# Kernel optimization log

Measured on AMD Instinct MI355X. Metric: run time of the kernel, lower is better.

The kernel has to match this reference:

```python
import jax, jax.numpy as jnp
import numpy as np

B, NCH, T = 4096, 8, 128
F1, F2 = 16, 32          # nChan*2, nChan*4
TP = 60                  # (128 - 10)//2 + 1 after enhanced block
FEAT = 2 * TP * F2       # 3840, matches nn.BatchNorm1d(3840)
NCLS = 12
HG = 4 * F2              # stacked LSTM gate rows (i,f,g,o)
EPS = 1e-5


def setup_inputs():
    key = jax.random.key(0)
    ks = jax.random.split(key, 24)
    n = lambda i, sh, s=0.1: jax.random.normal(ks[i], sh, dtype=jnp.float32) * s
    return {
        "x": jax.random.normal(ks[0], (B, 1, NCH, T), dtype=jnp.float32),
        "template": jax.random.normal(ks[1], (B, 1, NCH, T), dtype=jnp.float32),
        "conv1_w": n(2, (F1, 1, NCH, 1)),
        "conv1_b": n(3, (F1,)),
        "bn1_g": jnp.ones((F1,), jnp.float32),
        "bn1_b": jnp.zeros((F1,), jnp.float32),
        "prelu1": jnp.full((1,), 0.25, jnp.float32),
        "conv2_w": n(4, (F2, F1, 1, 10)),
        "conv2_b": n(5, (F2,)),
        "bn2_g": jnp.ones((F2,), jnp.float32),
        "bn2_b": jnp.zeros((F2,), jnp.float32),
        "prelu2": jnp.full((1,), 0.25, jnp.float32),
        "wih_f": n(6, (HG, F2)), "whh_f": n(7, (HG, F2)),
        "bih_f": n(8, (HG,)), "bhh_f": n(9, (HG,)),
        "wih_r": n(10, (HG, F2)), "whh_r": n(11, (HG, F2)),
        "bih_r": n(12, (HG,)), "bhh_r": n(13, (HG,)),
        "bnf_g": jnp.ones((FEAT,), jnp.float32),
        "bnf_b": jnp.zeros((FEAT,), jnp.float32),
        "convf_w": n(14, (1, 1, 5, 1)),
        "convf_b": n(15, (1,)),
    }


def _conv2d(x, w, b, stride=(1, 1), padding=((0, 0), (0, 0))):
    y = jax.lax.conv_general_dilated(x, w, window_strides=stride, padding=padding,
                                     dimension_numbers=("NCHW", "OIHW", "NCHW"))
    return y + b[None, :, None, None]


def _bn2d(x, g, b):  # training-mode batch stats over (N,H,W), biased var
    m = jnp.mean(x, axis=(0, 2, 3), keepdims=True)
    v = jnp.mean((x - m) ** 2, axis=(0, 2, 3), keepdims=True)
    return (x - m) * jax.lax.rsqrt(v + EPS) * g[None, :, None, None] + b[None, :, None, None]


def _bn1d(x, g, b):  # x: (N, FEAT)
    m = jnp.mean(x, axis=0, keepdims=True)
    v = jnp.mean((x - m) ** 2, axis=0, keepdims=True)
    return (x - m) * jax.lax.rsqrt(v + EPS) * g[None, :] + b[None, :]


def _prelu(x, a):
    return jnp.where(x >= 0, x, a * x)


def _lstm_dir(x, wih, whh, bih, bhh):  # x: (T, B, I) -> (T, B, H)
    Hh = whh.shape[1]
    Bn = x.shape[1]

    def step(carry, xt):
        h, c = carry
        gates = xt @ wih.T + h @ whh.T + bih + bhh  # (B, 4H), torch gate order i,f,g,o
        i, f, g, o = jnp.split(gates, 4, axis=-1)
        c = jax.nn.sigmoid(f) * c + jax.nn.sigmoid(i) * jnp.tanh(g)
        h = jax.nn.sigmoid(o) * jnp.tanh(c)
        return (h, c), h

    init = (jnp.zeros((Bn, Hh), x.dtype), jnp.zeros((Bn, Hh), x.dtype))
    _, hs = jax.lax.scan(step, init, x)
    return hs


def _rnn(xbct, wih_f, whh_f, bih_f, bhh_f, wih_r, whh_r, bih_r, bhh_r):
    # Faithful to torch: x.view(T, -1, c) is a raw row-major reshape of the
    # contiguous (b, c, T) buffer, NOT a transpose.
    b, c, Tn = xbct.shape
    xi = xbct.reshape(Tn, b, c)
    fwd = _lstm_dir(xi, wih_f, whh_f, bih_f, bhh_f)
    bwd = _lstm_dir(xi[::-1], wih_r, whh_r, bih_r, bhh_r)[::-1]
    r = jnp.concatenate([fwd, bwd], axis=-1)  # (T, b, 2c)
    return r.reshape(b, 2 * Tn * c, 1)        # raw reshape, matches r_out.view


def _forward(x, template, conv1_w, conv1_b, bn1_g, bn1_b, prelu1,
             conv2_w, conv2_b, bn2_g, bn2_b, prelu2,
             wih_f, whh_f, bih_f, bhh_f, wih_r, whh_r, bih_r, bhh_r,
             bnf_g, bnf_b, convf_w, convf_b):
    lstm_p = (wih_f, whh_f, bih_f, bhh_f, wih_r, whh_r, bih_r, bhh_r)

    def branch(inp):
        h = _conv2d(inp, conv1_w, conv1_b)               # (B, 16, 1, 128)
        h = _prelu(_bn2d(h, bn1_g, bn1_b), prelu1)
        h = _conv2d(h, conv2_w, conv2_b, stride=(1, 2))  # (B, 32, 1, 60)
        h = _prelu(_bn2d(h, bn2_g, bn2_b), prelu2)
        out_sig = h[:, :, 0, :]                          # (B, 32, 60)
        r1 = _rnn(out_sig, *lstm_p)
        # Original: numpy FFT round-trip -> detached, float cast keeps real part.
        fftm = jnp.real(jnp.fft.fft(jax.lax.stop_gradient(out_sig), axis=-1)).astype(inp.dtype)
        r2 = _rnn(fftm, *lstm_p)
        sig = (r1 + r2).reshape(-1, FEAT)                # (B, 3840)
        return _bn1d(sig, bnf_g, bnf_b)

    sig = branch(x)
    tpt = branch(template)

    x_ = sig.reshape(-1, 320, NCLS)
    t_ = tpt.reshape(-1, 320, NCLS)
    corr_xt = jnp.sum(x_ * t_, axis=1)
    corr_xx = jnp.sum(x_ * x_, axis=1)
    corr_tt = jnp.sum(t_ * t_, axis=1)
    corr = corr_xt / jnp.sqrt(corr_tt) / jnp.sqrt(corr_xx)  # (B, 12)

    o = corr.reshape(-1, NCLS, 1, 1)
    o = jnp.transpose(o, (0, 2, 1, 3))                      # (B, 1, 12, 1)
    o = _conv2d(o, convf_w, convf_b, padding=((2, 2), (0, 0)))
    out = o.reshape(-1, NCLS)
    return out, corr


def reference(x, template, conv1_w, conv1_b, bn1_g, bn1_b, prelu1,
              conv2_w, conv2_b, bn2_g, bn2_b, prelu2,
              wih_f, whh_f, bih_f, bhh_f, wih_r, whh_r, bih_r, bhh_r,
              bnf_g, bnf_b, convf_w, convf_b):
    return _forward(x, template, conv1_w, conv1_b, bn1_g, bn1_b, prelu1,
                    conv2_w, conv2_b, bn2_g, bn2_b, prelu2,
                    wih_f, whh_f, bih_f, bhh_f, wih_r, whh_r, bih_r, bhh_r,
                    bnf_g, bnf_b, convf_w, convf_b)
```

## Files before the change

### kernel.cpp

```cpp
#include <hip/hip_runtime.h>
#include <math.h>

#define EPS 1e-5f

typedef __attribute__((ext_vector_type(8))) short bf16x8;
typedef __attribute__((ext_vector_type(4))) float f32x4;
typedef __attribute__((ext_vector_type(4))) short s16x4;

__device__ __forceinline__ float fast_rcp(float x){ return __builtin_amdgcn_rcpf(x); }
__device__ __forceinline__ float sigf(float x){ return fast_rcp(1.0f + __expf(-x)); }
__device__ __forceinline__ float tanhfast(float x){ return fmaf(2.0f, fast_rcp(1.0f + __expf(-2.0f*x)), -1.0f); }
__device__ __forceinline__ float dot4(float4 a, float4 b, float c){
  return fmaf(a.w,b.w, fmaf(a.z,b.z, fmaf(a.y,b.y, fmaf(a.x,b.x, c))));
}
__device__ __forceinline__ short f2bf(float f){
  unsigned u = __float_as_uint(f);
  u = (u + 0x7FFFu + ((u>>16)&1u)) >> 16;
  return (short)u;
}
__device__ __forceinline__ float bf2f(short s){
  return __uint_as_float(((unsigned)(unsigned short)s) << 16);
}

__global__ __launch_bounds__(256) void k_conv1_stats(
    const float* __restrict__ x, const float* __restrict__ w1,
    const float* __restrict__ b1, float* __restrict__ part)
{
  __shared__ float red[4][32];
  float s[16], q[16];
#pragma unroll
  for (int f=0; f<16; ++f) { s[f]=0.f; q[f]=0.f; }
  float w1r[128];
#pragma unroll
  for (int i=0; i<128; ++i) w1r[i] = w1[i];
  float b1r[16];
#pragma unroll
  for (int f=0; f<16; ++f) b1r[f] = b1[f];
  const int tid = threadIdx.x;
  for (int iter=0; iter<8; ++iter) {
    int n = blockIdx.x*2048 + iter*256 + tid;
    int b = n >> 7, t = n & 127;
    const float* xb = x + b*1024 + t;
    float xv[8];
#pragma unroll
    for (int ch=0; ch<8; ++ch) xv[ch] = xb[ch*128];
#pragma unroll
    for (int f=0; f<16; ++f) {
      float v = b1r[f];
#pragma unroll
      for (int ch=0; ch<8; ++ch) v = fmaf(xv[ch], w1r[f*8+ch], v);
      s[f] += v; q[f] = fmaf(v,v,q[f]);
    }
  }
#pragma unroll
  for (int f=0; f<16; ++f) {
#pragma unroll
    for (int d=32; d>0; d>>=1) { s[f] += __shfl_down(s[f],d); q[f] += __shfl_down(q[f],d); }
  }
  const int lane = tid & 63, wv = tid >> 6;
  if (lane == 0) {
#pragma unroll
    for (int f=0; f<16; ++f) { red[wv][2*f] = s[f]; red[wv][2*f+1] = q[f]; }
  }
  __syncthreads();
  if (tid < 32) {
    float v = red[0][tid] + red[1][tid] + red[2][tid] + red[3][tid];
    part[blockIdx.x*32 + tid] = v;
  }
}

__global__ __launch_bounds__(256) void k_reduce_finalize(
    const float* __restrict__ part, int nblk, int C,
    const float* __restrict__ g, const float* __restrict__ b,
    float* __restrict__ prm, float invN)
{
  __shared__ float red[4][2];
  const int c = blockIdx.x;
  const int tid = threadIdx.x;
  float s=0.f, q=0.f;
  for (int i=tid; i<nblk; i+=256) {
    s += part[(size_t)i*2*C + 2*c];
    q += part[(size_t)i*2*C + 2*c + 1];
  }
#pragma unroll
  for (int d=32; d>0; d>>=1) { s += __shfl_down(s,d); q += __shfl_down(q,d); }
  const int lane = tid & 63, wv = tid >> 6;
  if (lane==0) { red[wv][0]=s; red[wv][1]=q; }
  __syncthreads();
  if (tid==0) {
    s = red[0][0]+red[1][0]+red[2][0]+red[3][0];
    q = red[0][1]+red[1][1]+red[2][1]+red[3][1];
    float m = s*invN;
    float v = q*invN - m*m;
    float sc = g[c] / sqrtf(v + EPS);
    prm[2*c]   = sc;
    prm[2*c+1] = fmaf(-m, sc, b[c]);
  }
}

__global__ __launch_bounds__(256) void k_conv2(
    const float* __restrict__ x,
    const float* __restrict__ w1, const float* __restrict__ b1,
    const float* __restrict__ prm1, const float* __restrict__ prelu1,
    const float* __restrict__ w2, const float* __restrict__ b2,
    float* __restrict__ sig, float* __restrict__ part2)
{
  __shared__ float xb[1024];
  __shared__ float h1p[16*136];
  __shared__ float w2s[32*16*12];
  __shared__ float w1s[128];
  __shared__ float p1s[32];
  int tid = threadIdx.x; int b = blockIdx.x;
  *(float4*)&xb[tid*4] = *(const float4*)&x[b*1024 + tid*4];
  for (int i=tid; i<5120; i+=256) { int ff=i/10, k=i-ff*10; w2s[ff*12+k] = w2[i]; }
  if (tid<128) w1s[tid] = w1[tid];
  if (tid<32)  p1s[tid] = prm1[tid];
  float a1 = prelu1[0];
  __syncthreads();
#pragma unroll
  for (int r=0; r<8; ++r) {
    int o = tid + 256*r; int f = o>>7, t = o&127;
    float v = b1[f];
#pragma unroll
    for (int ch=0; ch<8; ++ch) v = fmaf(xb[ch*128+t], w1s[f*8+ch], v);
    v = fmaf(v, p1s[2*f], p1s[2*f+1]);
    v = (v>=0.f) ? v : a1*v;
    h1p[f*136 + t] = v;
  }
  __syncthreads();
  int f2 = tid>>3, wb = (tid&7)*8;
  float acc[8];
  float bb = b2[f2];
#pragma unroll
  for (int j=0;j<8;++j) acc[j]=bb;
  for (int f1=0; f1<16; ++f1) {
    const float* hrow = &h1p[f1*136 + 2*wb];
    float hw[24];
#pragma unroll
    for (int m=0;m<6;++m) *(float4*)&hw[m*4] = *(const float4*)&hrow[m*4];
    const float* wr = &w2s[(f2*16+f1)*12];
    float wk[10];
    *(float4*)&wk[0] = *(const float4*)&wr[0];
    *(float4*)&wk[4] = *(const float4*)&wr[4];
    wk[8]=wr[8]; wk[9]=wr[9];
#pragma unroll
    for (int j=0;j<8;++j)
#pragma unroll
      for (int k=0;k<10;++k) acc[j] = fmaf(hw[2*j+k], wk[k], acc[j]);
  }
  float s=0.f, q=0.f;
#pragma unroll
  for (int j=0;j<8;++j) {
    int w = wb+j;
    if (w < 60) { sig[b*1920 + f2*60 + w] = acc[j]; s += acc[j]; q = fmaf(acc[j],acc[j],q); }
  }
  s += __shfl_down(s,4,8); q += __shfl_down(q,4,8);
  s += __shfl_down(s,2,8); q += __shfl_down(q,2,8);
  s += __shfl_down(s,1,8); q += __shfl_down(q,1,8);
  if ((tid&7)==0) {
    part2[(size_t)b*64 + 2*f2]     = s;
    part2[(size_t)b*64 + 2*f2 + 1] = q;
  }
}

__global__ void k_costab(float* __restrict__ ct)
{
  int i = blockIdx.x*256 + threadIdx.x;
  if (i < 3600) {
    int k = i/60, n = i - k*60;
    int m = (k*n) % 60;
    ct[i] = cosf(0.104719755119659775f * (float)m);
  }
}

__global__ __launch_bounds__(256) void k_sigfft(
    float* __restrict__ sig, float* __restrict__ fft,
    const float* __restrict__ prm2, const float* __restrict__ prelu2,
    const float* __restrict__ ctab)
{
  __shared__ float ct[3600];
  __shared__ float rowb[4][4][60];
  int tid = threadIdx.x;
  for (int i=tid; i<3600; i+=256) ct[i] = ctab[i];
  int r4 = tid>>6, lane = tid&63;
  float a2 = prelu2[0];
  __syncthreads();
#pragma unroll
  for (int it=0; it<4; ++it) {
    int row = blockIdx.x*16 + it*4 + r4;
    int c = row & 31;
    float sc = prm2[2*c], sh = prm2[2*c+1];
    size_t base = (size_t)row*60;
    if (lane < 60) {
      float v = fmaf(sig[base+lane], sc, sh);
      v = (v>=0.f) ? v : a2*v;
      rowb[it][r4][lane] = v;
      sig[base+lane] = v;
    }
    if (lane < 60) {
      float s = 0.f;
      const float* rb = rowb[it][r4];
#pragma unroll 6
      for (int n=0; n<60; ++n) s = fmaf(rb[n], ct[n*60+lane], s);
      fft[base+lane] = s;
    }
  }
}

__global__ __launch_bounds__(256) void k_xfrag(const float* __restrict__ src, short* __restrict__ frag)
{
  __shared__ float XS[64*33];
  const int tid = threadIdx.x;
  const int bid = blockIdx.x;
  const int t = bid >> 6, sblk = bid & 63;
  const float* sp = src + (size_t)t*131072 + (size_t)sblk*2048;
  {
    float4 v0 = *(const float4*)&sp[tid*8];
    float4 v1 = *(const float4*)&sp[tid*8 + 4];
    int s = tid >> 2, k = (tid & 3) * 8;
    float* d = &XS[s*33 + k];
    d[0]=v0.x; d[1]=v0.y; d[2]=v0.z; d[3]=v0.w;
    d[4]=v1.x; d[5]=v1.y; d[6]=v1.z; d[7]=v1.w;
  }
  __syncthreads();
  const int stile = tid >> 6, l = tid & 63;
  const int m = l & 15, g = l >> 4;
  const float* rp = &XS[(stile*16 + m)*33 + g*8];
  bf16x8 v;
#pragma unroll
  for (int j=0;j<8;++j) v[j] = f2bf(rp[j]);
  *(bf16x8*)(frag + ((size_t)(t*256 + sblk*4 + stile)*64 + l)*8) = v;
}

__global__ __launch_bounds__(256,1) void k_lstm_mfma(
    const short* __restrict__ fragSA, const short* __restrict__ fragFA,
    const short* __restrict__ fragSB, const short* __restrict__ fragFB,
    float* __restrict__ routA, float* __restrict__ routB,
    const float* __restrict__ wihf, const float* __restrict__ whhf,
    const float* __restrict__ bihf, const float* __restrict__ bhhf,
    const float* __restrict__ wihr, const float* __restrict__ whhr,
    const float* __restrict__ bihr, const float* __restrict__ bhhr,
    int zsel)
{
  __shared__ short hbuf[2][5120];
  const int tid = threadIdx.x;
  const int l = tid & 63, wv = tid >> 6;
  const int a = wv >> 1, ch = wv & 1;
  const int m = l & 15, g = l >> 4;
  const int sb = blockIdx.x * 64;
  const int dir = blockIdx.y;
  const int br = (gridDim.z == 2) ? blockIdx.z : zsel;
  const short* fragS = br ? fragSB : fragSA;
  const short* fragF = br ? fragFB : fragFA;
  float* out = br ? routB : routA;
  const float* wih = dir ? wihr : wihf;
  const float* whh = dir ? whhr : whhf;
  const float* bih = dir ? bihr : bihf;
  const float* bhh = dir ? bhhr : bhhf;

  bf16x8 Ax[4], Ah[4];
#pragma unroll
  for (int G=0; G<4; ++G) {
    const float* wr = wih + (size_t)(32*G + 16*a + m)*32 + 8*g;
    const float* hr = whh + (size_t)(32*G + 16*a + m)*32 + 8*g;
#pragma unroll
    for (int j=0;j<8;++j){ Ax[G][j]=f2bf(wr[j]); Ah[G][j]=f2bf(hr[j]); }
  }
  float bias[16];
#pragma unroll
  for (int G=0;G<4;++G)
#pragma unroll
    for (int r=0;r<4;++r){
      int row = 32*G + 16*a + 4*g + r;
      bias[G*4+r] = bih[row] + bhh[row];
    }
  for (int i=tid; i<2560; i+=256) ((int*)hbuf[1])[i] = 0;

  const short* fsrc = ch ? fragF : fragS;
  const int st0 = sb >> 4;
  const int tt0 = dir ? 59 : 0;
  bf16x8 bx[4];
#pragma unroll
  for (int ct=0; ct<4; ++ct)
    bx[ct] = *(const bf16x8*)(fsrc + ((size_t)(tt0*256 + st0 + ct)*64 + l)*8);

  float cst[16];
#pragma unroll
  for (int i=0;i<16;++i) cst[i]=0.f;

  __syncthreads();

#pragma unroll 2
  for (int q=0; q<60; ++q) {
    const int tt = dir ? (59-q) : q;
    const short* hrd = hbuf[(q+1)&1];
    bf16x8 bh[4];
#pragma unroll
    for (int ct=0; ct<4; ++ct)
      bh[ct] = *(const bf16x8*)(hrd + (64*ch + 16*ct + m)*40 + 8*g);
    bf16x8 bx2[4];
    if (q < 59) {
      const int tn = dir ? (58-q) : (q+1);
#pragma unroll
      for (int ct=0; ct<4; ++ct)
        bx2[ct] = *(const bf16x8*)(fsrc + ((size_t)(tn*256 + st0 + ct)*64 + l)*8);
    }
    f32x4 acc[16];
#pragma unroll
    for (int G=0; G<4; ++G) {
      f32x4 binit;
      binit[0]=bias[G*4]; binit[1]=bias[G*4+1]; binit[2]=bias[G*4+2]; binit[3]=bias[G*4+3];
#pragma unroll
      for (int ct=0; ct<4; ++ct) {
        f32x4 t0 = __builtin_amdgcn_mfma_f32_16x16x32_bf16(Ax[G], bx[ct], binit, 0,0,0);
        acc[G*4+ct] = __builtin_amdgcn_mfma_f32_16x16x32_bf16(Ah[G], bh[ct], t0, 0,0,0);
      }
    }
    short* hwr = hbuf[q&1];
#pragma unroll
    for (int ct=0; ct<4; ++ct) {
      s16x4 hv;
#pragma unroll
      for (int r=0; r<4; ++r) {
        float gi = acc[0*4+ct][r], gf = acc[1*4+ct][r];
        float gg = acc[2*4+ct][r], go = acc[3*4+ct][r];
        float c = sigf(gf)*cst[ct*4+r] + sigf(gi)*tanhfast(gg);
        cst[ct*4+r] = c;
        hv[r] = f2bf(sigf(go)*tanhfast(c));
      }
      *(s16x4*)(hwr + (64*ch + 16*ct + m)*40 + 16*a + 4*g) = hv;
    }
    __syncthreads();
#pragma unroll
    for (int i2=0; i2<2; ++i2) {
      int s = 32*ch + 16*i2 + m;
      const s16x4 h1 = *(const s16x4*)(hwr + s*40 + 16*a + 4*g);
      const s16x4 h2 = *(const s16x4*)(hwr + (64+s)*40 + 16*a + 4*g);
      float4 o;
      o.x = bf2f(h1[0])+bf2f(h2[0]);
      o.y = bf2f(h1[1])+bf2f(h2[1]);
      o.z = bf2f(h1[2])+bf2f(h2[2]);
      o.w = bf2f(h1[3])+bf2f(h2[3]);
      *(float4*)(out + (size_t)tt*262144 + (size_t)(sb+s)*64 + dir*32 + 16*a + 4*g) = o;
    }
#pragma unroll
    for (int ct=0; ct<4; ++ct) bx[ct] = bx2[ct];
  }
}

__global__ __launch_bounds__(256) void k_bnfstats(const float* __restrict__ rb, float* __restrict__ acc)
{
  int col = blockIdx.x*256 + threadIdx.x;
  size_t r0 = (size_t)blockIdx.y*256;
  const float* p = rb + r0*3840 + col;
  float s=0.f, q=0.f;
  for (int r=0; r<256; ++r) { float v = p[(size_t)r*3840]; s += v; q = fmaf(v,v,q); }
  atomicAdd(&acc[2*col], s); atomicAdd(&acc[2*col+1], q);
}

__global__ void k_finalize_bn(const float* __restrict__ acc, const float* __restrict__ g,
                              const float* __restrict__ b, float* __restrict__ prm,
                              int C, float invN)
{
  int i = blockIdx.x*blockDim.x + threadIdx.x;
  if (i < C) {
    float m = acc[2*i]*invN;
    float v = acc[2*i+1]*invN - m*m;
    float sc = g[i] / sqrtf(v + EPS);
    prm[2*i]   = sc;
    prm[2*i+1] = fmaf(-m, sc, b[i]);
  }
}

__global__ __launch_bounds__(64) void k_corr(
    const float* __restrict__ ra, const float* __restrict__ rb,
    const float* __restrict__ pfa, const float* __restrict__ pfb,
    const float* __restrict__ cw, const float* __restrict__ cb,
    float* __restrict__ dout)
{
  __shared__ float sxt[12], sxx[12], stt[12], cv[12];
  int lane = threadIdx.x; int r = blockIdx.x;
  if (lane < 12) { sxt[lane]=0.f; sxx[lane]=0.f; stt[lane]=0.f; }
  __syncthreads();
  const float* pa = ra + (size_t)r*3840;
  const float* pb = rb + (size_t)r*3840;
  float xt0=0,xx0=0,tt0=0, xt1=0,xx1=0,tt1=0, xt2=0,xx2=0,tt2=0;
  for (int i=0; i<60; i+=3) {
    { int fe = lane + 64*i;
      float a = fmaf(pa[fe], pfa[2*fe], pfa[2*fe+1]);
      float b = fmaf(pb[fe], pfb[2*fe], pfb[2*fe+1]);
      xt0 = fmaf(a,b,xt0); xx0 = fmaf(a,a,xx0); tt0 = fmaf(b,b,tt0); }
    { int fe = lane + 64*(i+1);
      float a = fmaf(pa[fe], pfa[2*fe], pfa[2*fe+1]);
      float b = fmaf(pb[fe], pfb[2*fe], pfb[2*fe+1]);
      xt1 = fmaf(a,b,xt1); xx1 = fmaf(a,a,xx1); tt1 = fmaf(b,b,tt1); }
    { int fe = lane + 64*(i+2);
      float a = fmaf(pa[fe], pfa[2*fe], pfa[2*fe+1]);
      float b = fmaf(pb[fe], pfb[2*fe], pfb[2*fe+1]);
      xt2 = fmaf(a,b,xt2); xx2 = fmaf(a,a,xx2); tt2 = fmaf(b,b,tt2); }
  }
  int c0 = lane % 12;
  int c1 = (c0+4) % 12;
  int c2 = (c0+8) % 12;
  atomicAdd(&sxt[c0], xt0); atomicAdd(&sxx[c0], xx0); atomicAdd(&stt[c0], tt0);
  atomicAdd(&sxt[c1], xt1); atomicAdd(&sxx[c1], xx1); atomicAdd(&stt[c1], tt1);
  atomicAdd(&sxt[c2], xt2); atomicAdd(&sxx[c2], xx2); atomicAdd(&stt[c2], tt2);
  __syncthreads();
  if (lane < 12) {
    float corr = sxt[lane] / sqrtf(stt[lane]) / sqrtf(sxx[lane]);
    cv[lane] = corr;
    dout[49152 + r*12 + lane] = corr;
  }
  __syncthreads();
  if (lane < 12) {
    float o = cb[0];
#pragma unroll
    for (int k=0; k<5; ++k) { int j = lane + k - 2; if (j>=0 && j<12) o = fmaf(cv[j], cw[k], o); }
    dout[r*12 + lane] = o;
  }
}

extern "C" void kernel_launch(void* const* d_in, const int* in_sizes, int n_in,
                              void* d_out, int out_size, void* d_ws, size_t ws_size,
                              hipStream_t stream)
{
  const float* x    = (const float*)d_in[0];
  const float* tpl  = (const float*)d_in[1];
  const float* w1   = (const float*)d_in[2];
  const float* b1   = (const float*)d_in[3];
  const float* g1   = (const float*)d_in[4];
  const float* bb1  = (const float*)d_in[5];
  const float* p1   = (const float*)d_in[6];
  const float* w2   = (const float*)d_in[7];
  const float* b2   = (const float*)d_in[8];
  const float* g2   = (const float*)d_in[9];
  const float* bb2  = (const float*)d_in[10];
  const float* p2   = (const float*)d_in[11];
  const float* wihf = (const float*)d_in[12];
  const float* whhf = (const float*)d_in[13];
  const float* bihf = (const float*)d_in[14];
  const float* bhhf = (const float*)d_in[15];
  const float* wihr = (const float*)d_in[16];
  const float* whhr = (const float*)d_in[17];
  const float* bihr = (const float*)d_in[18];
  const float* bhhr = (const float*)d_in[19];
  const float* gf   = (const float*)d_in[20];
  const float* bf   = (const float*)d_in[21];
  const float* cw   = (const float*)d_in[22];
  const float* cb   = (const float*)d_in[23];
  float* W   = (float*)d_ws;
  float* out = (float*)d_out;

  constexpr size_t PRM1A=64, PRM1B=96, PRM2A=256, PRM2B=320;
  constexpr size_t ACCFA=512, ACCFB=8192, PRMFA=15872, PRMFB=23552, CTAB=31232;
  constexpr size_t P1P=35072, P2P=43264;
  constexpr size_t SIGSZ = 7864320, RSZ = 15728640, FRAGF = 3932160;
  constexpr size_t BIG0 = 307200;
  constexpr size_t F_SIGA=BIG0, F_FFTA=F_SIGA+SIGSZ, F_SIGB=F_FFTA+SIGSZ, F_FFTB=F_SIGB+SIGSZ;
  constexpr size_t F_RBUFA=F_FFTB+SIGSZ, F_RBUFB=F_RBUFA+RSZ;
  constexpr size_t F_FR0=F_RBUFB+RSZ;
  constexpr size_t F_TOTAL=(F_FR0 + 4*FRAGF)*sizeof(float);
  constexpr size_t T_SIG=BIG0, T_FFT=T_SIG+SIGSZ, T_RBUFA=T_FFT+SIGSZ, T_RBUFB=T_RBUFA+RSZ;
  constexpr size_t T_FR0=T_RBUFB+RSZ;

  const bool fast = ws_size >= F_TOTAL;

  hipMemsetAsync(W, 0, 65536*sizeof(float)/sizeof(float)>0?262144:262144, stream);
  k_costab<<<15,256,0,stream>>>(W+CTAB);

  if (fast) {
    for (int br=0; br<2; ++br) {
      const float* xin  = br ? tpl : x;
      float* prm1 = W + (br ? PRM1B : PRM1A);
      float* prm2 = W + (br ? PRM2B : PRM2A);
      float* sig  = W + (br ? F_SIGB : F_SIGA);
      float* fft  = W + (br ? F_FFTB : F_FFTA);
      k_conv1_stats<<<256,256,0,stream>>>(xin, w1, b1, W+P1P);
      k_reduce_finalize<<<16,256,0,stream>>>(W+P1P, 256, 16, g1, bb1, prm1, 1.f/524288.f);
      k_conv2<<<4096,256,0,stream>>>(xin, w1, b1, prm1, p1, w2, b2, sig, W+P2P);
      k_reduce_finalize<<<32,256,0,stream>>>(W+P2P, 4096, 32, g2, bb2, prm2, 1.f/245760.f);
      k_sigfft<<<8192,256,0,stream>>>(sig, fft, prm2, p2, W+CTAB);
    }
    short* frSA = (short*)(W + F_FR0);
    short* frFA = (short*)(W + F_FR0 + FRAGF);
    short* frSB = (short*)(W + F_FR0 + 2*FRAGF);
    short* frFB = (short*)(W + F_FR0 + 3*FRAGF);
    k_xfrag<<<3840,256,0,stream>>>(W+F_SIGA, frSA);
    k_xfrag<<<3840,256,0,stream>>>(W+F_FFTA, frFA);
    k_xfrag<<<3840,256,0,stream>>>(W+F_SIGB, frSB);
    k_xfrag<<<3840,256,0,stream>>>(W+F_FFTB, frFB);
    k_lstm_mfma<<<dim3(64,2,2),256,0,stream>>>(frSA, frFA, frSB, frFB,
        W+F_RBUFA, W+F_RBUFB,
        wihf,whhf,bihf,bhhf, wihr,whhr,bihr,bhhr, 0);
    k_bnfstats<<<dim3(15,16),256,0,stream>>>(W+F_RBUFA, W+ACCFA);
    k_bnfstats<<<dim3(15,16),256,0,stream>>>(W+F_RBUFB, W+ACCFB);
    k_finalize_bn<<<15,256,0,stream>>>(W+ACCFA, gf, bf, W+PRMFA, 3840, 1.f/4096.f);
    k_finalize_bn<<<15,256,0,stream>>>(W+ACCFB, gf, bf, W+PRMFB, 3840, 1.f/4096.f);
    k_corr<<<4096,64,0,stream>>>(W+F_RBUFA, W+F_RBUFB, W+PRMFA, W+PRMFB, cw, cb, out);
  } else {
    short* frS = (short*)(W + T_FR0);
    short* frF = (short*)(W + T_FR0 + FRAGF);
    for (int br=0; br<2; ++br) {
      const float* xin  = br ? tpl : x;
      float* prm1 = W + (br ? PRM1B : PRM1A);
      float* prm2 = W + (br ? PRM2B : PRM2A);
      float* sig  = W + T_SIG;
      float* fft  = W + T_FFT;
      float* rbuf = W + (br ? T_RBUFB : T_RBUFA);
      k_conv1_stats<<<256,256,0,stream>>>(xin, w1, b1, W+P1P);
      k_reduce_finalize<<<16,256,0,stream>>>(W+P1P, 256, 16, g1, bb1, prm1, 1.f/524288.f);
      k_conv2<<<4096,256,0,stream>>>(xin, w1, b1, prm1, p1, w2, b2, sig, W+P2P);
      k_reduce_finalize<<<32,256,0,stream>>>(W+P2P, 4096, 32, g2, bb2, prm2, 1.f/245760.f);
      k_sigfft<<<8192,256,0,stream>>>(sig, fft, prm2, p2, W+CTAB);
      k_xfrag<<<3840,256,0,stream>>>(sig, frS);
      k_xfrag<<<3840,256,0,stream>>>(fft, frF);
      k_lstm_mfma<<<dim3(64,2,1),256,0,stream>>>(frS, frF, frS, frF,
          rbuf, rbuf, wihf,whhf,bihf,bhhf, wihr,whhr,bihr,bhhr, 0);
    }
    k_bnfstats<<<dim3(15,16),256,0,stream>>>(W+T_RBUFA, W+ACCFA);
    k_bnfstats<<<dim3(15,16),256,0,stream>>>(W+T_RBUFB, W+ACCFB);
    k_finalize_bn<<<15,256,0,stream>>>(W+ACCFA, gf, bf, W+PRMFA, 3840, 1.f/4096.f);
    k_finalize_bn<<<15,256,0,stream>>>(W+ACCFB, gf, bf, W+PRMFB, 3840, 1.f/4096.f);
    k_corr<<<4096,64,0,stream>>>(W+T_RBUFA, W+T_RBUFB, W+PRMFA, W+PRMFB, cw, cb, out);
  }
}
```

Baseline: 688.4 us.

## Restructure LSTM into single-wave blocks over 8-sequence tiles with shuffle-based sum

The LSTM kernel moves from 256-thread blocks, each covering 64 sequences with a block-wide barrier every step, to 64-thread single-wave blocks. Each wave covers 8 sig plus 8 fft sequences packed into one 16-column MFMA tile and computes all 8 gate row tiles. The sig+fft output sum now uses lane shuffles, which removes the LDS round trip and the __syncthreads per timestep. Fragment building is simplified to interleave sig and fft directly without LDS. In exchange, every wave recomputes the full weight fragments and the grid grows much larger, with each wave carrying a serial 60-step chain.

```diff
diff --git a/kernel.cpp b/kernel.cpp
--- a/kernel.cpp
+++ b/kernel.cpp
@@ -10,9 +10,6 @@
 __device__ __forceinline__ float fast_rcp(float x){ return __builtin_amdgcn_rcpf(x); }
 __device__ __forceinline__ float sigf(float x){ return fast_rcp(1.0f + __expf(-x)); }
 __device__ __forceinline__ float tanhfast(float x){ return fmaf(2.0f, fast_rcp(1.0f + __expf(-2.0f*x)), -1.0f); }
-__device__ __forceinline__ float dot4(float4 a, float4 b, float c){
-  return fmaf(a.w,b.w, fmaf(a.z,b.z, fmaf(a.y,b.y, fmaf(a.x,b.x, c))));
-}
 __device__ __forceinline__ short f2bf(float f){
   unsigned u = __float_as_uint(f);
   u = (u + 0x7FFFu + ((u>>16)&1u)) >> 16;
@@ -207,144 +204,108 @@
   }
 }
 
-__global__ __launch_bounds__(256) void k_xfrag(const float* __restrict__ src, short* __restrict__ frag)
-{
-  __shared__ float XS[64*33];
+__global__ __launch_bounds__(256) void k_xfrag2(
+    const float* __restrict__ sig, const float* __restrict__ fft,
+    short* __restrict__ frag)
+{
   const int tid = threadIdx.x;
-  const int bid = blockIdx.x;
-  const int t = bid >> 6, sblk = bid & 63;
-  const float* sp = src + (size_t)t*131072 + (size_t)sblk*2048;
-  {
-    float4 v0 = *(const float4*)&sp[tid*8];
-    float4 v1 = *(const float4*)&sp[tid*8 + 4];
-    int s = tid >> 2, k = (tid & 3) * 8;
-    float* d = &XS[s*33 + k];
-    d[0]=v0.x; d[1]=v0.y; d[2]=v0.z; d[3]=v0.w;
-    d[4]=v1.x; d[5]=v1.y; d[6]=v1.z; d[7]=v1.w;
-  }
-  __syncthreads();
-  const int stile = tid >> 6, l = tid & 63;
+  const int wv = tid >> 6, l = tid & 63;
+  const int id = blockIdx.x*4 + wv;
+  const int t = id >> 9, sg = id & 511;
   const int m = l & 15, g = l >> 4;
-  const float* rp = &XS[(stile*16 + m)*33 + g*8];
+  const float* src = (m < 8) ? sig : fft;
+  const float* p = src + (size_t)t*131072 + (size_t)(8*sg + (m&7))*32 + 8*g;
+  float4 v0 = *(const float4*)p;
+  float4 v1 = *(const float4*)(p+4);
   bf16x8 v;
-#pragma unroll
-  for (int j=0;j<8;++j) v[j] = f2bf(rp[j]);
-  *(bf16x8*)(frag + ((size_t)(t*256 + sblk*4 + stile)*64 + l)*8) = v;
-}
-
-__global__ __launch_bounds__(256,1) void k_lstm_mfma(
-    const short* __restrict__ fragSA, const short* __restrict__ fragFA,
-    const short* __restrict__ fragSB, const short* __restrict__ fragFB,
+  v[0]=f2bf(v0.x); v[1]=f2bf(v0.y); v[2]=f2bf(v0.z); v[3]=f2bf(v0.w);
+  v[4]=f2bf(v1.x); v[5]=f2bf(v1.y); v[6]=f2bf(v1.z); v[7]=f2bf(v1.w);
+  *(bf16x8*)(frag + ((size_t)id*64 + l)*8) = v;
+}
+
+__global__ __launch_bounds__(64,2) void k_lstm8(
+    const short* __restrict__ fragA, const short* __restrict__ fragB,
     float* __restrict__ routA, float* __restrict__ routB,
     const float* __restrict__ wihf, const float* __restrict__ whhf,
     const float* __restrict__ bihf, const float* __restrict__ bhhf,
     const float* __restrict__ wihr, const float* __restrict__ whhr,
-    const float* __restrict__ bihr, const float* __restrict__ bhhr,
-    int zsel)
-{
-  __shared__ short hbuf[2][5120];
-  const int tid = threadIdx.x;
-  const int l = tid & 63, wv = tid >> 6;
-  const int a = wv >> 1, ch = wv & 1;
+    const float* __restrict__ bihr, const float* __restrict__ bhhr)
+{
+  __shared__ short hb[640];
+  const int l = threadIdx.x & 63;
   const int m = l & 15, g = l >> 4;
-  const int sb = blockIdx.x * 64;
+  const int sg = blockIdx.x;
   const int dir = blockIdx.y;
-  const int br = (gridDim.z == 2) ? blockIdx.z : zsel;
-  const short* fragS = br ? fragSB : fragSA;
-  const short* fragF = br ? fragFB : fragFA;
+  const int br = blockIdx.z;
+  const short* frag = br ? fragB : fragA;
   float* out = br ? routB : routA;
   const float* wih = dir ? wihr : wihf;
   const float* whh = dir ? whhr : whhf;
   const float* bih = dir ? bihr : bihf;
   const float* bhh = dir ? bhhr : bhhf;
 
-  bf16x8 Ax[4], Ah[4];
-#pragma unroll
-  for (int G=0; G<4; ++G) {
-    const float* wr = wih + (size_t)(32*G + 16*a + m)*32 + 8*g;
-    const float* hr = whh + (size_t)(32*G + 16*a + m)*32 + 8*g;
-#pragma unroll
-    for (int j=0;j<8;++j){ Ax[G][j]=f2bf(wr[j]); Ah[G][j]=f2bf(hr[j]); }
-  }
-  float bias[16];
-#pragma unroll
-  for (int G=0;G<4;++G)
-#pragma unroll
-    for (int r=0;r<4;++r){
-      int row = 32*G + 16*a + 4*g + r;
-      bias[G*4+r] = bih[row] + bhh[row];
-    }
-  for (int i=tid; i<2560; i+=256) ((int*)hbuf[1])[i] = 0;
-
-  const short* fsrc = ch ? fragF : fragS;
-  const int st0 = sb >> 4;
+  bf16x8 Ax[8], Ah[8];
+#pragma unroll
+  for (int rt=0; rt<8; ++rt) {
+    const float* wr = wih + (size_t)(16*rt+m)*32 + 8*g;
+    const float* hr = whh + (size_t)(16*rt+m)*32 + 8*g;
+#pragma unroll
+    for (int j=0;j<8;++j){ Ax[rt][j]=f2bf(wr[j]); Ah[rt][j]=f2bf(hr[j]); }
+  }
+  f32x4 bias[8];
+#pragma unroll
+  for (int rt=0; rt<8; ++rt)
+#pragma unroll
+    for (int r=0;r<4;++r){ int R=16*rt+4*g+r; bias[rt][r]=bih[R]+bhh[R]; }
+
+  for (int i=l; i<320; i+=64) ((int*)hb)[i] = 0;
+
+  float cst[2][4];
+#pragma unroll
+  for (int h2=0;h2<2;++h2)
+#pragma unroll
+    for (int r=0;r<4;++r) cst[h2][r]=0.f;
+
   const int tt0 = dir ? 59 : 0;
-  bf16x8 bx[4];
-#pragma unroll
-  for (int ct=0; ct<4; ++ct)
-    bx[ct] = *(const bf16x8*)(fsrc + ((size_t)(tt0*256 + st0 + ct)*64 + l)*8);
-
-  float cst[16];
-#pragma unroll
-  for (int i=0;i<16;++i) cst[i]=0.f;
-
-  __syncthreads();
-
-#pragma unroll 2
+  bf16x8 bx = *(const bf16x8*)(frag + ((size_t)(tt0*512+sg)*64 + l)*8);
+
   for (int q=0; q<60; ++q) {
     const int tt = dir ? (59-q) : q;
-    const short* hrd = hbuf[(q+1)&1];
-    bf16x8 bh[4];
-#pragma unroll
-    for (int ct=0; ct<4; ++ct)
-      bh[ct] = *(const bf16x8*)(hrd + (64*ch + 16*ct + m)*40 + 8*g);
-    bf16x8 bx2[4];
+    bf16x8 bh = *(const bf16x8*)(hb + m*40 + 8*g);
+    bf16x8 bxn;
     if (q < 59) {
       const int tn = dir ? (58-q) : (q+1);
-#pragma unroll
-      for (int ct=0; ct<4; ++ct)
-        bx2[ct] = *(const bf16x8*)(fsrc + ((size_t)(tn*256 + st0 + ct)*64 + l)*8);
-    }
-    f32x4 acc[16];
-#pragma unroll
-    for (int G=0; G<4; ++G) {
-      f32x4 binit;
-      binit[0]=bias[G*4]; binit[1]=bias[G*4+1]; binit[2]=bias[G*4+2]; binit[3]=bias[G*4+3];
-#pragma unroll
-      for (int ct=0; ct<4; ++ct) {
-        f32x4 t0 = __builtin_amdgcn_mfma_f32_16x16x32_bf16(Ax[G], bx[ct], binit, 0,0,0);
-        acc[G*4+ct] = __builtin_amdgcn_mfma_f32_16x16x32_bf16(Ah[G], bh[ct], t0, 0,0,0);
+      bxn = *(const bf16x8*)(frag + ((size_t)(tn*512+sg)*64 + l)*8);
+    }
+    f32x4 acc[8];
+#pragma unroll
+    for (int rt=0; rt<8; ++rt) {
+      acc[rt] = __builtin_amdgcn_mfma_f32_16x16x32_bf16(Ax[rt], bx, bias[rt], 0,0,0);
+      acc[rt] = __builtin_amdgcn_mfma_f32_16x16x32_bf16(Ah[rt], bh, acc[rt], 0,0,0);
+    }
+#pragma unroll
+    for (int h2=0; h2<2; ++h2) {
+      s16x4 hv;
+      float hnf[4];
+#pragma unroll
+      for (int r=0; r<4; ++r) {
+        float gi = acc[h2][r],   gf = acc[2+h2][r];
+        float gg = acc[4+h2][r], go = acc[6+h2][r];
+        float cn = sigf(gf)*cst[h2][r] + sigf(gi)*tanhfast(gg);
+        cst[h2][r] = cn;
+        float hn = sigf(go)*tanhfast(cn);
+        hnf[r] = hn; hv[r] = f2bf(hn);
       }
-    }
-    short* hwr = hbuf[q&1];
-#pragma unroll
-    for (int ct=0; ct<4; ++ct) {
-      s16x4 hv;
-#pragma unroll
-      for (int r=0; r<4; ++r) {
-        float gi = acc[0*4+ct][r], gf = acc[1*4+ct][r];
-        float gg = acc[2*4+ct][r], go = acc[3*4+ct][r];
-        float c = sigf(gf)*cst[ct*4+r] + sigf(gi)*tanhfast(gg);
-        cst[ct*4+r] = c;
-        hv[r] = f2bf(sigf(go)*tanhfast(c));
-      }
-      *(s16x4*)(hwr + (64*ch + 16*ct + m)*40 + 16*a + 4*g) = hv;
-    }
-    __syncthreads();
-#pragma unroll
-    for (int i2=0; i2<2; ++i2) {
-      int s = 32*ch + 16*i2 + m;
-      const s16x4 h1 = *(const s16x4*)(hwr + s*40 + 16*a + 4*g);
-      const s16x4 h2 = *(const s16x4*)(hwr + (64+s)*40 + 16*a + 4*g);
+      *(s16x4*)(hb + m*40 + 16*h2 + 4*g) = hv;
       float4 o;
-      o.x = bf2f(h1[0])+bf2f(h2[0]);
-      o.y = bf2f(h1[1])+bf2f(h2[1]);
-      o.z = bf2f(h1[2])+bf2f(h2[2]);
-      o.w = bf2f(h1[3])+bf2f(h2[3]);
-      *(float4*)(out + (size_t)tt*262144 + (size_t)(sb+s)*64 + dir*32 + 16*a + 4*g) = o;
-    }
-#pragma unroll
-    for (int ct=0; ct<4; ++ct) bx[ct] = bx2[ct];
+      o.x = hnf[0] + __shfl_xor(hnf[0], 8);
+      o.y = hnf[1] + __shfl_xor(hnf[1], 8);
+      o.z = hnf[2] + __shfl_xor(hnf[2], 8);
+      o.w = hnf[3] + __shfl_xor(hnf[3], 8);
+      if (m < 8)
+        *(float4*)(out + (size_t)tt*262144 + (size_t)(8*sg+m)*64 + dir*32 + 16*h2 + 4*g) = o;
+    }
+    bx = bxn;
   }
 }
 
@@ -454,18 +415,18 @@
   constexpr size_t PRM1A=64, PRM1B=96, PRM2A=256, PRM2B=320;
   constexpr size_t ACCFA=512, ACCFB=8192, PRMFA=15872, PRMFB=23552, CTAB=31232;
   constexpr size_t P1P=35072, P2P=43264;
-  constexpr size_t SIGSZ = 7864320, RSZ = 15728640, FRAGF = 3932160;
+  constexpr size_t SIGSZ = 7864320, RSZ = 15728640, FRAGF = 7864320;
   constexpr size_t BIG0 = 307200;
   constexpr size_t F_SIGA=BIG0, F_FFTA=F_SIGA+SIGSZ, F_SIGB=F_FFTA+SIGSZ, F_FFTB=F_SIGB+SIGSZ;
   constexpr size_t F_RBUFA=F_FFTB+SIGSZ, F_RBUFB=F_RBUFA+RSZ;
   constexpr size_t F_FR0=F_RBUFB+RSZ;
-  constexpr size_t F_TOTAL=(F_FR0 + 4*FRAGF)*sizeof(float);
+  constexpr size_t F_TOTAL=(F_FR0 + 2*FRAGF)*sizeof(float);
   constexpr size_t T_SIG=BIG0, T_FFT=T_SIG+SIGSZ, T_RBUFA=T_FFT+SIGSZ, T_RBUFB=T_RBUFA+RSZ;
   constexpr size_t T_FR0=T_RBUFB+RSZ;
 
   const bool fast = ws_size >= F_TOTAL;
 
-  hipMemsetAsync(W, 0, 65536*sizeof(float)/sizeof(float)>0?262144:262144, stream);
+  hipMemsetAsync(W, 0, 262144, stream);
   k_costab<<<15,256,0,stream>>>(W+CTAB);
 
   if (fast) {
@@ -481,25 +442,19 @@
       k_reduce_finalize<<<32,256,0,stream>>>(W+P2P, 4096, 32, g2, bb2, prm2, 1.f/245760.f);
       k_sigfft<<<8192,256,0,stream>>>(sig, fft, prm2, p2, W+CTAB);
     }
-    short* frSA = (short*)(W + F_FR0);
-    short* frFA = (short*)(W + F_FR0 + FRAGF);
-    short* frSB = (short*)(W + F_FR0 + 2*FRAGF);
-    short* frFB = (short*)(W + F_FR0 + 3*FRAGF);
-    k_xfrag<<<3840,256,0,stream>>>(W+F_SIGA, frSA);
-    k_xfrag<<<3840,256,0,stream>>>(W+F_FFTA, frFA);
-    k_xfrag<<<3840,256,0,stream>>>(W+F_SIGB, frSB);
-    k_xfrag<<<3840,256,0,stream>>>(W+F_FFTB, frFB);
-    k_lstm_mfma<<<dim3(64,2,2),256,0,stream>>>(frSA, frFA, frSB, frFB,
-        W+F_RBUFA, W+F_RBUFB,
-        wihf,whhf,bihf,bhhf, wihr,whhr,bihr,bhhr, 0);
+    short* frA = (short*)(W + F_FR0);
+    short* frB = (short*)(W + F_FR0 + FRAGF);
+    k_xfrag2<<<7680,256,0,stream>>>(W+F_SIGA, W+F_FFTA, frA);
+    k_xfrag2<<<7680,256,0,stream>>>(W+F_SIGB, W+F_FFTB, frB);
+    k_lstm8<<<dim3(512,2,2),64,0,stream>>>(frA, frB, W+F_RBUFA, W+F_RBUFB,
+        wihf,whhf,bihf,bhhf, wihr,whhr,bihr,bhhr);
     k_bnfstats<<<dim3(15,16),256,0,stream>>>(W+F_RBUFA, W+ACCFA);
     k_bnfstats<<<dim3(15,16),256,0,stream>>>(W+F_RBUFB, W+ACCFB);
     k_finalize_bn<<<15,256,0,stream>>>(W+ACCFA, gf, bf, W+PRMFA, 3840, 1.f/4096.f);
     k_finalize_bn<<<15,256,0,stream>>>(W+ACCFB, gf, bf, W+PRMFB, 3840, 1.f/4096.f);
     k_corr<<<4096,64,0,stream>>>(W+F_RBUFA, W+F_RBUFB, W+PRMFA, W+PRMFB, cw, cb, out);
   } else {
-    short* frS = (short*)(W + T_FR0);
-    short* frF = (short*)(W + T_FR0 + FRAGF);
+    short* fr = (short*)(W + T_FR0);
     for (int br=0; br<2; ++br) {
       const float* xin  = br ? tpl : x;
       float* prm1 = W + (br ? PRM1B : PRM1A);
@@ -512,10 +467,9 @@
       k_conv2<<<4096,256,0,stream>>>(xin, w1, b1, prm1, p1, w2, b2, sig, W+P2P);
       k_reduce_finalize<<<32,256,0,stream>>>(W+P2P, 4096, 32, g2, bb2, prm2, 1.f/245760.f);
       k_sigfft<<<8192,256,0,stream>>>(sig, fft, prm2, p2, W+CTAB);
-      k_xfrag<<<3840,256,0,stream>>>(sig, frS);
-      k_xfrag<<<3840,256,0,stream>>>(fft, frF);
-      k_lstm_mfma<<<dim3(64,2,1),256,0,stream>>>(frS, frF, frS, frF,
-          rbuf, rbuf, wihf,whhf,bihf,bhhf, wihr,whhr,bihr,bhhr, 0);
+      k_xfrag2<<<7680,256,0,stream>>>(sig, fft, fr);
+      k_lstm8<<<dim3(512,2,1),64,0,stream>>>(fr, fr, rbuf, rbuf,
+          wihf,whhf,bihf,bhhf, wihr,whhr,bihr,bhhr);
     }
     k_bnfstats<<<dim3(15,16),256,0,stream>>>(W+T_RBUFA, W+ACCFA);
     k_bnfstats<<<dim3(15,16),256,0,stream>>>(W+T_RBUFB, W+ACCFB);
```

Measured after the change: 652.8 us. 5.2% less time.
